# Optimization experiments

Measured on AMD Instinct MI355X. Metric: run time of the kernel, lower is better.

The kernel has to match this reference:

```python
import jax, jax.numpy as jnp
import numpy as np
from jax import lax

V, E, T, F, K = 100000, 300, 50, 100, 3
B, S = 32, 512


def setup_inputs() -> dict:
    key = jax.random.key(0)
    ks = jax.random.split(key, 10)
    inp = {
        "x": jax.random.randint(ks[0], (B, S), 0, V),
        "tags": jax.random.randint(ks[1], (B, S), 0, T),
        "emb": jax.random.normal(ks[2], (V, E), dtype=jnp.float32),
        "conv_w": jax.random.normal(ks[3], (F, E, K), dtype=jnp.float32) / np.sqrt(E * K),
        "conv_b": jnp.zeros((F,), dtype=jnp.float32),
        "fc_w": jax.random.normal(ks[4], (T, F), dtype=jnp.float32) / np.sqrt(F),
        "fc_b": jnp.zeros((T,), dtype=jnp.float32),
        "start_trans": jax.random.uniform(ks[5], (T,), dtype=jnp.float32, minval=-0.1, maxval=0.1),
        "end_trans": jax.random.uniform(ks[6], (T,), dtype=jnp.float32, minval=-0.1, maxval=0.1),
        "trans": jax.random.uniform(ks[7], (T, T), dtype=jnp.float32, minval=-0.1, maxval=0.1),
    }
    return inp


def _emissions(x, emb, conv_w, conv_b, fc_w, fc_b):
    e = emb[x]                                   # [B,S,E] embedding gather
    e = jnp.transpose(e, (0, 2, 1))              # [B,E,S]
    h = lax.conv_general_dilated(e, conv_w, (1,), [(K // 2, K // 2)])  # [B,F,S] (NCW/OIW)
    h = jax.nn.relu(h + conv_b[None, :, None])   # dropout is identity in eval
    feat = jnp.transpose(h, (0, 2, 1))           # [B,S,F]
    return (jnp.einsum("bsf,tf->bst", feat, fc_w) + fc_b).astype(jnp.float32)  # [B,S,T]


def _crf_nll(emissions, tags, start_trans, end_trans, trans):
    # numerator: score of the gold tag path (full mask)
    em_tag = jnp.take_along_axis(emissions, tags[..., None], axis=-1)[..., 0]  # [B,S]
    num = (start_trans[tags[:, 0]]
           + em_tag.sum(-1)
           + trans[tags[:, :-1], tags[:, 1:]].sum(-1)
           + end_trans[tags[:, -1]])                                           # [B]

    # denominator: forward algorithm via scan over time
    alpha0 = start_trans[None, :] + emissions[:, 0]                             # [B,T]

    def step(alpha, em_t):
        # alpha: [B,T] prev scores; em_t: [B,T] emissions at t
        new = jax.nn.logsumexp(alpha[:, :, None] + trans[None] + em_t[:, None, :], axis=1)
        return new, None

    alpha, _ = lax.scan(step, alpha0, jnp.transpose(emissions[:, 1:], (1, 0, 2)))
    log_z = jax.nn.logsumexp(alpha + end_trans[None, :], axis=-1)               # [B]
    return -(num - log_z).sum()  # torchcrf default reduction='sum'; model returns -llh


def reference(x, tags, emb, conv_w, conv_b, fc_w, fc_b, start_trans, end_trans, trans):
    emissions = _emissions(x, emb, conv_w, conv_b, fc_w, fc_b)
    return _crf_nll(emissions, tags, start_trans, end_trans, trans)
```

## Files before the change

### kernel.cpp

```cpp
#include <hip/hip_runtime.h>
#include <hip/hip_bf16.h>
#include <math.h>

#define BB 32
#define SS 512
#define EE 300
#define FF 100
#define TT 50
#define CH 16
#define NC 32

typedef __attribute__((ext_vector_type(8))) short v8s;
typedef __attribute__((ext_vector_type(4))) float v4f;
#define MFMA16 __builtin_amdgcn_mfma_f32_16x16x32_bf16

#define AP 328
#define BKC 160
#define A2P 136
#define MP 72

__device__ inline unsigned short f2bf(float v) {
    unsigned u = __float_as_uint(v);
    unsigned r = u + 0x7fff + ((u >> 16) & 1);
    return (unsigned short)(r >> 16);
}
__device__ inline float bf2f(short s) {
    return __uint_as_float(((unsigned)(unsigned short)s) << 16);
}
__device__ inline v8s ldsld8(const short* p) {
    return *(const v8s*)__builtin_assume_aligned(p, 16);
}
__device__ inline void g2lds16(const void* g, void* l) {
    __builtin_amdgcn_global_load_lds(
        (const __attribute__((address_space(1))) unsigned int*)g,
        (__attribute__((address_space(3))) unsigned int*)l, 16, 0, 0);
}

__global__ void prep_kernel(const float* __restrict__ tr, const float* __restrict__ cw,
                            const float* __restrict__ fcw,
                            unsigned short* __restrict__ wB2,
                            unsigned short* __restrict__ fcwT2,
                            unsigned short* __restrict__ AT,
                            unsigned short* __restrict__ Ab)
{
    const int gid = blockIdx.x * 256 + threadIdx.x;
    const int gs  = 64 * 256;
    for (int idx = gid; idx < 6 * 128 * BKC; idx += gs) {
        int c = idx / (128 * BKC); int r = idx - c * 128 * BKC;
        int f = r / BKC; int j = r - f * BKC;
        int gk = c * BKC + j; int kk = gk / 320; int e = gk - kk * 320;
        float v = (f < FF && e < EE) ? cw[f * 900 + e * 3 + kk] : 0.f;
        wB2[idx] = f2bf(v);
    }
    for (int idx = gid; idx < 64 * A2P; idx += gs) {
        int t = idx / A2P, f = idx - t * A2P;
        float v = (t < TT && f < FF) ? fcw[t * FF + f] : 0.f;
        fcwT2[idx] = f2bf(v);
    }
    for (int idx = gid; idx < 64 * 64; idx += gs) {
        int r = idx >> 6, c2 = idx & 63;
        AT[idx] = (r < TT && c2 < TT) ? f2bf(__expf(tr[c2 * TT + r])) : 0;
        Ab[idx] = (r < TT && c2 < TT) ? f2bf(__expf(tr[r * TT + c2])) : 0;
    }
}

__global__ __launch_bounds__(256, 2) void emis_kernel(
    const int* __restrict__ x, const float* __restrict__ emb,
    const unsigned short* __restrict__ wB2, const float* __restrict__ cb,
    const unsigned short* __restrict__ fcwT2, const float* __restrict__ fcb,
    const int* __restrict__ tags,
    float* __restrict__ expem, float* __restrict__ rmv, float* __restrict__ emtag)
{
    __shared__ __align__(16) short ldsA[34 * AP];
    __shared__ __align__(16) short ldsB[128 * BKC];

    const int b   = blockIdx.y;
    const int s0  = blockIdx.x * 32;
    const int tid = threadIdx.x;
    const int wv  = tid >> 6;
    const int lane = tid & 63;
    const int col = lane & 15;
    const int q   = lane >> 4;

    for (int g = tid; g < 34 * 75; g += 256) {
        int r = g / 75, eg = g - r * 75; int e0 = eg * 4;
        int gsq = s0 - 1 + r;
        short4 o;
        if (gsq >= 0 && gsq < SS) {
            int xr = x[b * SS + gsq];
            const float4 v = *(const float4*)(emb + (size_t)xr * EE + e0);
            o = make_short4((short)f2bf(v.x), (short)f2bf(v.y),
                            (short)f2bf(v.z), (short)f2bf(v.w));
        } else o = make_short4(0, 0, 0, 0);
        *(short4*)&ldsA[r * AP + e0] = o;
    }
    if (tid < 34 * 5) {
        int r = tid / 5, c0 = 300 + (tid % 5) * 4;
        *(short4*)&ldsA[r * AP + c0] = make_short4(0, 0, 0, 0);
    }

    v4f acc[2][2];
#pragma unroll
    for (int a = 0; a < 2; ++a)
#pragma unroll
        for (int f = 0; f < 2; ++f) acc[a][f] = (v4f){0.f, 0.f, 0.f, 0.f};

    const int ftA = wv * 2, ftB = wv * 2 + 1;
    for (int ch = 0; ch < 6; ++ch) {
        const char* gsrc = (const char*)(wB2 + (size_t)ch * 128 * BKC);
#pragma unroll
        for (int it = 0; it < 10; ++it) {
            int seg = it * 4 + wv;
            g2lds16(gsrc + seg * 1024 + lane * 16, (char*)ldsB + seg * 1024);
        }
        __syncthreads();
#pragma unroll
        for (int sl = 0; sl < 5; ++sl) {
            int gk = ch * BKC + sl * 32;
            int kk = gk / 320;
            int e0 = gk - kk * 320;
            v8s a0 = ldsld8(&ldsA[(col + kk) * AP + e0 + q * 8]);
            v8s a1 = ldsld8(&ldsA[(16 + col + kk) * AP + e0 + q * 8]);
            v8s b0 = ldsld8(&ldsB[(ftA * 16 + col) * BKC + sl * 32 + q * 8]);
            v8s b1 = ldsld8(&ldsB[(ftB * 16 + col) * BKC + sl * 32 + q * 8]);
            acc[0][0] = MFMA16(a0, b0, acc[0][0], 0, 0, 0);
            acc[0][1] = MFMA16(a0, b1, acc[0][1], 0, 0, 0);
            acc[1][0] = MFMA16(a1, b0, acc[1][0], 0, 0, 0);
            acc[1][1] = MFMA16(a1, b1, acc[1][1], 0, 0, 0);
        }
        __syncthreads();
    }

    short* A2 = ldsB;
    short* B2 = ldsB + 32 * A2P;
#pragma unroll
    for (int st = 0; st < 2; ++st)
#pragma unroll
        for (int fi = 0; fi < 2; ++fi) {
            int f = (wv * 2 + fi) * 16 + col;
            float bias = (f < FF) ? cb[f] : 0.f;
#pragma unroll
            for (int rg = 0; rg < 4; ++rg) {
                int s = st * 16 + q * 4 + rg;
                float v = (f < FF) ? fmaxf(acc[st][fi][rg] + bias, 0.f) : 0.f;
                A2[s * A2P + f] = (short)f2bf(v);
            }
        }
#pragma unroll
    for (int it = 0; it < 5; ++it) {
        int seg = it * 4 + wv;
        if (seg < 17) g2lds16((const char*)fcwT2 + seg * 1024 + lane * 16,
                              (char*)B2 + seg * 1024);
    }
    __syncthreads();

    if (wv < 2) {
        v4f a2[4];
#pragma unroll
        for (int nt = 0; nt < 4; ++nt) a2[nt] = (v4f){0.f, 0.f, 0.f, 0.f};
#pragma unroll
        for (int ks = 0; ks < 4; ++ks) {
            v8s af = ldsld8(&A2[(wv * 16 + col) * A2P + ks * 32 + q * 8]);
#pragma unroll
            for (int nt = 0; nt < 4; ++nt) {
                v8s bt = ldsld8(&B2[(nt * 16 + col) * A2P + ks * 32 + q * 8]);
                a2[nt] = MFMA16(af, bt, a2[nt], 0, 0, 0);
            }
        }
        float fb0 = fcb[col], fb1 = fcb[16 + col], fb2 = fcb[32 + col];
        float fb3 = (col < 2) ? fcb[48 + col] : 0.f;
#pragma unroll
        for (int rg = 0; rg < 4; ++rg) {
            int s = s0 + wv * 16 + q * 4 + rg;
            float e0v = a2[0][rg] + fb0;
            float e1v = a2[1][rg] + fb1;
            float e2v = a2[2][rg] + fb2;
            float e3v = (col < 2) ? a2[3][rg] + fb3 : -1e30f;
            float m = fmaxf(fmaxf(e0v, e1v), fmaxf(e2v, e3v));
#pragma unroll
            for (int off = 1; off < 16; off <<= 1) m = fmaxf(m, __shfl_xor(m, off));
            int gidx = b * SS + s;
            if (col == 0) rmv[gidx] = m;
            int tg = tags[gidx];
            float* orow = expem + (size_t)gidx * TT;
            orow[col]      = __expf(e0v - m);
            orow[16 + col] = __expf(e1v - m);
            orow[32 + col] = __expf(e2v - m);
            if (col < 2) orow[48 + col] = __expf(e3v - m);
            if (tg == col)            emtag[gidx] = e0v;
            else if (tg == 16 + col)  emtag[gidx] = e1v;
            else if (tg == 32 + col)  emtag[gidx] = e2v;
            else if (col < 2 && tg == 48 + col) emtag[gidx] = e3v;
        }
    }
}

__global__ __launch_bounds__(64) void chunk_kernel(
    const float* __restrict__ expem, const unsigned short* __restrict__ AT,
    const unsigned short* __restrict__ Ab,
    unsigned short* __restrict__ R, float* __restrict__ lsR)
{
    __shared__ __align__(16) short L[2][64 * MP];
    __shared__ __align__(16) float emL[CH][64];
    const int c = blockIdx.x, b = blockIdx.y;
    const int lane = threadIdx.x;
    const int col = lane & 15, q = lane >> 4;
    const int t0 = c * CH + 1;
    const int nf = (c == NC - 1) ? (SS - 1 - (NC - 1) * CH) : CH;

    for (int idx = lane; idx < CH * 64; idx += 64) {
        int k = idx >> 6, m = idx & 63;
        float v = 0.f;
        if (m < TT && k < nf) v = expem[((size_t)(b * SS + t0 + k)) * TT + m];
        emL[k][m] = v;
    }

    v8s af[4][2];
#pragma unroll
    for (int jt = 0; jt < 4; ++jt)
#pragma unroll
        for (int kc = 0; kc < 2; ++kc)
            af[jt][kc] = *(const v8s*)(AT + (jt * 16 + col) * 64 + kc * 32 + q * 8);
    __syncthreads();

    {
        const v8s* arow = (const v8s*)(Ab + lane * 64);
#pragma unroll
        for (int g = 0; g < 8; ++g) {
            v8s a = arow[g];
            v8s o;
#pragma unroll
            for (int e = 0; e < 8; ++e)
                o[e] = (short)f2bf(bf2f(a[e]) * emL[0][g * 8 + e]);
            *(v8s*)&L[0][lane * MP + g * 8] = o;
        }
    }

    int cur = 0;
    for (int k = 1; k < nf; ++k) {
        __syncthreads();
        v8s bf[4][2];
#pragma unroll
        for (int nt = 0; nt < 4; ++nt)
#pragma unroll
            for (int kc = 0; kc < 2; ++kc)
                bf[nt][kc] = ldsld8(&L[cur][(nt * 16 + col) * MP + kc * 32 + q * 8]);
        v4f acc[4][4];
#pragma unroll
        for (int jt = 0; jt < 4; ++jt)
#pragma unroll
            for (int nt = 0; nt < 4; ++nt) {
                acc[jt][nt] = (v4f){0.f, 0.f, 0.f, 0.f};
                acc[jt][nt] = MFMA16(af[jt][0], bf[nt][0], acc[jt][nt], 0, 0, 0);
                acc[jt][nt] = MFMA16(af[jt][1], bf[nt][1], acc[jt][nt], 0, 0, 0);
            }
        if (k < nf - 1) {
#pragma unroll
            for (int jt = 0; jt < 4; ++jt) {
                const float4 em4 = *(const float4*)&emL[k][jt * 16 + q * 4];
#pragma unroll
                for (int nt = 0; nt < 4; ++nt) {
                    short4 o;
                    o.x = (short)f2bf(acc[jt][nt][0] * em4.x);
                    o.y = (short)f2bf(acc[jt][nt][1] * em4.y);
                    o.z = (short)f2bf(acc[jt][nt][2] * em4.z);
                    o.w = (short)f2bf(acc[jt][nt][3] * em4.w);
                    *(short4*)&L[cur ^ 1][(nt * 16 + col) * MP + jt * 16 + q * 4] = o;
                }
            }
            cur ^= 1;
        } else {
            float vals[4][4][4];
            float mx = 0.f;
#pragma unroll
            for (int jt = 0; jt < 4; ++jt) {
                const float4 em4 = *(const float4*)&emL[k][jt * 16 + q * 4];
#pragma unroll
                for (int nt = 0; nt < 4; ++nt) {
                    vals[jt][nt][0] = acc[jt][nt][0] * em4.x;
                    vals[jt][nt][1] = acc[jt][nt][1] * em4.y;
                    vals[jt][nt][2] = acc[jt][nt][2] * em4.z;
                    vals[jt][nt][3] = acc[jt][nt][3] * em4.w;
#pragma unroll
                    for (int r = 0; r < 4; ++r) mx = fmaxf(mx, vals[jt][nt][r]);
                }
            }
#pragma unroll
            for (int off = 1; off < 64; off <<= 1) mx = fmaxf(mx, __shfl_xor(mx, off));
            mx = fmaxf(mx, 1e-37f);
            float inv = 1.f / mx;
            unsigned short* Rc = R + ((size_t)(b * NC + c) << 12);
#pragma unroll
            for (int jt = 0; jt < 4; ++jt)
#pragma unroll
                for (int nt = 0; nt < 4; ++nt)
#pragma unroll
                    for (int r = 0; r < 4; ++r)
                        Rc[(jt * 16 + q * 4 + r) * 64 + nt * 16 + col] =
                            f2bf(vals[jt][nt][r] * inv);
            if (lane == 0) lsR[b * NC + c] = __logf(mx);
        }
    }
}

__global__ __launch_bounds__(64) void chain_kernel(
    const float* __restrict__ expem, const unsigned short* __restrict__ R,
    const float* __restrict__ lsR, const float* __restrict__ start,
    const float* __restrict__ endt, float* __restrict__ lzpart)
{
    __shared__ __align__(16) float pvec[64];
    const int b = blockIdx.x, i = threadIdx.x;

    pvec[i] = (i < TT) ? __expf(start[i]) * expem[((size_t)(b * SS)) * TT + i] : 0.f;

    const unsigned short* Rb = R + ((size_t)(b * NC) << 12);
    v8s rowb[8];
#pragma unroll
    for (int g = 0; g < 8; ++g) rowb[g] = *(const v8s*)(Rb + i * 64 + g * 8);
    float logacc = 0.f;
    __syncthreads();

    for (int c = 0; c < NC; ++c) {
        float rw[64];
#pragma unroll
        for (int g = 0; g < 8; ++g)
#pragma unroll
            for (int e = 0; e < 8; ++e) rw[g * 8 + e] = bf2f(rowb[g][e]);
        if (c + 1 < NC) {
            const unsigned short* Rn = Rb + ((size_t)(c + 1) << 12);
#pragma unroll
            for (int g = 0; g < 8; ++g) rowb[g] = *(const v8s*)(Rn + i * 64 + g * 8);
        }
        float acc = 0.f;
        const float4* pv = (const float4*)pvec;
#pragma unroll
        for (int g = 0; g < 16; ++g) {
            float4 p4 = pv[g];
            acc = fmaf(rw[g * 4 + 0], p4.x, acc);
            acc = fmaf(rw[g * 4 + 1], p4.y, acc);
            acc = fmaf(rw[g * 4 + 2], p4.z, acc);
            acc = fmaf(rw[g * 4 + 3], p4.w, acc);
        }
        float mx = acc;
#pragma unroll
        for (int off = 1; off < 64; off <<= 1) mx = fmaxf(mx, __shfl_xor(mx, off));
        mx = fmaxf(mx, 1e-37f);
        logacc += __logf(mx) + lsR[b * NC + c];
        __syncthreads();
        pvec[i] = acc * (1.f / mx);
        __syncthreads();
    }

    float sv = (i < TT) ? pvec[i] * __expf(endt[i]) : 0.f;
#pragma unroll
    for (int off = 1; off < 64; off <<= 1) sv += __shfl_xor(sv, off);
    if (i == 0) lzpart[b] = logacc + __logf(sv);
}

__global__ __launch_bounds__(256) void final_kernel(
    const float* __restrict__ emtag, const float* __restrict__ rmv,
    const int* __restrict__ tags, const float* __restrict__ tr,
    const float* __restrict__ start, const float* __restrict__ endt,
    const float* __restrict__ lzpart, float* __restrict__ out)
{
    __shared__ float redN[256], redR[256], nllsh[BB];
    const int tid = threadIdx.x;
    const int b   = tid >> 3;
    const int sl  = tid & 7;
    const int base = b * SS + sl * 64;

    float accN = 0.f, accR = 0.f;
    for (int k = 0; k < 64; ++k) {
        int s = sl * 64 + k;
        accN += emtag[base + k];
        accR += rmv[base + k];
        int tg = tags[base + k];
        if (s < SS - 1) accN += tr[tg * TT + tags[base + k + 1]];
    }
    redN[tid] = accN; redR[tid] = accR;
    __syncthreads();

    if (sl == 0) {
        float tn = 0.f, trm = 0.f;
#pragma unroll
        for (int k = 0; k < 8; ++k) { tn += redN[b * 8 + k]; trm += redR[b * 8 + k]; }
        float num = tn + start[tags[b * SS]] + endt[tags[b * SS + SS - 1]];
        float lz  = trm + lzpart[b];
        nllsh[b] = lz - num;
    }
    __syncthreads();
    if (tid < 64) {
        float v = (tid < BB) ? nllsh[tid] : 0.f;
#pragma unroll
        for (int off = 1; off < 64; off <<= 1) v += __shfl_xor(v, off);
        if (tid == 0) out[0] = v;
    }
}

extern "C" void kernel_launch(void* const* d_in, const int* in_sizes, int n_in,
                              void* d_out, int out_size, void* d_ws, size_t ws_size,
                              hipStream_t stream)
{
    const int*   x    = (const int*)d_in[0];
    const int*   tags = (const int*)d_in[1];
    const float* emb  = (const float*)d_in[2];
    const float* cw   = (const float*)d_in[3];
    const float* cb   = (const float*)d_in[4];
    const float* fcw  = (const float*)d_in[5];
    const float* fcb  = (const float*)d_in[6];
    const float* st   = (const float*)d_in[7];
    const float* en   = (const float*)d_in[8];
    const float* tr   = (const float*)d_in[9];

    unsigned short* wB2   = (unsigned short*)d_ws;
    unsigned short* fcwT2 = wB2 + 6 * 128 * BKC;
    unsigned short* ATm   = fcwT2 + 64 * A2P;
    unsigned short* Abm   = ATm + 4096;
    unsigned short* Rm    = Abm + 4096;
    float* fbase  = (float*)(Rm + (size_t)BB * NC * 4096);
    float* expem  = fbase;
    float* rmv    = expem + (size_t)BB * SS * TT;
    float* emtag  = rmv + BB * SS;
    float* lsR    = emtag + BB * SS;
    float* lzpart = lsR + BB * NC;

    prep_kernel<<<dim3(64), 256, 0, stream>>>(tr, cw, fcw, wB2, fcwT2, ATm, Abm);
    emis_kernel<<<dim3(16, BB), 256, 0, stream>>>(x, emb, wB2, cb, fcwT2, fcb,
                                                  tags, expem, rmv, emtag);
    chunk_kernel<<<dim3(NC, BB), 64, 0, stream>>>(expem, ATm, Abm, Rm, lsR);
    chain_kernel<<<dim3(BB), 64, 0, stream>>>(expem, Rm, lsR, st, en, lzpart);
    final_kernel<<<dim3(1), 256, 0, stream>>>(emtag, rmv, tags, tr, st, en,
                                              lzpart, (float*)d_out);
}
```

Measured before the change: 256.5 us.

## Double-buffer conv weights in MFMA layout and fuse numerator into chain kernel

```diff
diff --git a/kernel.cpp b/kernel.cpp
--- a/kernel.cpp
+++ b/kernel.cpp
@@ -15,8 +15,10 @@
 #define MFMA16 __builtin_amdgcn_mfma_f32_16x16x32_bf16
 
 #define AP 328
-#define BKC 160
-#define A2P 136
+#define NCH 10
+#define CKS 3
+#define CHB (128 * 96)
+#define A2P 152
 #define MP 72
 
 __device__ inline unsigned short f2bf(float v) {
@@ -45,15 +47,22 @@
 {
     const int gid = blockIdx.x * 256 + threadIdx.x;
     const int gs  = 64 * 256;
-    for (int idx = gid; idx < 6 * 128 * BKC; idx += gs) {
-        int c = idx / (128 * BKC); int r = idx - c * 128 * BKC;
-        int f = r / BKC; int j = r - f * BKC;
-        int gk = c * BKC + j; int kk = gk / 320; int e = gk - kk * 320;
-        float v = (f < FF && e < EE) ? cw[f * 900 + e * 3 + kk] : 0.f;
+    for (int idx = gid; idx < NCH * CKS * 8 * 512; idx += gs) {
+        int e = idx & 7, p = (idx >> 3) & 63, blk = idx >> 9;
+        int ch = blk / 24, rem = blk - ch * 24;
+        int sl = rem >> 3, ft = rem & 7;
+        int col = p >> 2, q = p & 3;
+        int n  = ft * 16 + col;
+        int gk = ch * 96 + sl * 32 + q * 8 + e;
+        int kk = gk / 320, ee = gk - kk * 320;
+        float v = (n < FF && ee < EE) ? cw[n * 900 + ee * 3 + kk] : 0.f;
         wB2[idx] = f2bf(v);
     }
-    for (int idx = gid; idx < 64 * A2P; idx += gs) {
-        int t = idx / A2P, f = idx - t * A2P;
+    for (int idx = gid; idx < 16 * 512; idx += gs) {
+        int e = idx & 7, p = (idx >> 3) & 63, blk = idx >> 9;
+        int ks = blk >> 2, nt = blk & 3;
+        int col = p >> 2, q = p & 3;
+        int t = nt * 16 + col, f = ks * 32 + q * 8 + e;
         float v = (t < TT && f < FF) ? fcw[t * FF + f] : 0.f;
         fcwT2[idx] = f2bf(v);
     }
@@ -72,15 +81,23 @@
     float* __restrict__ expem, float* __restrict__ rmv, float* __restrict__ emtag)
 {
     __shared__ __align__(16) short ldsA[34 * AP];
-    __shared__ __align__(16) short ldsB[128 * BKC];
-
-    const int b   = blockIdx.y;
-    const int s0  = blockIdx.x * 32;
-    const int tid = threadIdx.x;
-    const int wv  = tid >> 6;
+    __shared__ __align__(16) short ldsB[2][CHB];
+
+    const int b    = blockIdx.y;
+    const int s0   = blockIdx.x * 32;
+    const int tid  = threadIdx.x;
+    const int wv   = tid >> 6;
     const int lane = tid & 63;
-    const int col = lane & 15;
-    const int q   = lane >> 4;
+    const int col  = lane & 15;
+    const int q    = lane >> 4;
+    const int bofs = ((col << 2) | q) << 3;
+
+#pragma unroll
+    for (int it = 0; it < 6; ++it) {
+        int seg = it * 4 + wv;
+        g2lds16((const char*)wB2 + seg * 1024 + lane * 16,
+                (char*)ldsB[0] + seg * 1024);
+    }
 
     for (int g = tid; g < 34 * 75; g += 256) {
         int r = g / 75, eg = g - r * 75; int e0 = eg * 4;
@@ -98,6 +115,7 @@
         int r = tid / 5, c0 = 300 + (tid % 5) * 4;
         *(short4*)&ldsA[r * AP + c0] = make_short4(0, 0, 0, 0);
     }
+    __syncthreads();
 
     v4f acc[2][2];
 #pragma unroll
@@ -106,23 +124,26 @@
         for (int f = 0; f < 2; ++f) acc[a][f] = (v4f){0.f, 0.f, 0.f, 0.f};
 
     const int ftA = wv * 2, ftB = wv * 2 + 1;
-    for (int ch = 0; ch < 6; ++ch) {
-        const char* gsrc = (const char*)(wB2 + (size_t)ch * 128 * BKC);
-#pragma unroll
-        for (int it = 0; it < 10; ++it) {
-            int seg = it * 4 + wv;
-            g2lds16(gsrc + seg * 1024 + lane * 16, (char*)ldsB + seg * 1024);
-        }
-        __syncthreads();
-#pragma unroll
-        for (int sl = 0; sl < 5; ++sl) {
-            int gk = ch * BKC + sl * 32;
-            int kk = gk / 320;
+    for (int ch = 0; ch < NCH; ++ch) {
+        if (ch < NCH - 1) {
+            const char* g = (const char*)(wB2 + (size_t)(ch + 1) * CHB);
+            char* l = (char*)ldsB[(ch + 1) & 1];
+#pragma unroll
+            for (int it = 0; it < 6; ++it) {
+                int seg = it * 4 + wv;
+                g2lds16(g + seg * 1024 + lane * 16, l + seg * 1024);
+            }
+        }
+        const short* Bc = ldsB[ch & 1];
+#pragma unroll
+        for (int sl = 0; sl < CKS; ++sl) {
+            int gk = ch * 96 + sl * 32;
+            int kk = (gk >= 640) ? 2 : (gk >= 320 ? 1 : 0);
             int e0 = gk - kk * 320;
             v8s a0 = ldsld8(&ldsA[(col + kk) * AP + e0 + q * 8]);
             v8s a1 = ldsld8(&ldsA[(16 + col + kk) * AP + e0 + q * 8]);
-            v8s b0 = ldsld8(&ldsB[(ftA * 16 + col) * BKC + sl * 32 + q * 8]);
-            v8s b1 = ldsld8(&ldsB[(ftB * 16 + col) * BKC + sl * 32 + q * 8]);
+            v8s b0 = ldsld8(&Bc[((sl * 8 + ftA) << 9) + bofs]);
+            v8s b1 = ldsld8(&Bc[((sl * 8 + ftB) << 9) + bofs]);
             acc[0][0] = MFMA16(a0, b0, acc[0][0], 0, 0, 0);
             acc[0][1] = MFMA16(a0, b1, acc[0][1], 0, 0, 0);
             acc[1][0] = MFMA16(a1, b0, acc[1][0], 0, 0, 0);
@@ -131,8 +152,14 @@
         __syncthreads();
     }
 
-    short* A2 = ldsB;
-    short* B2 = ldsB + 32 * A2P;
+    short* A2 = ldsB[0];
+    short* B2 = ldsB[1];
+#pragma unroll
+    for (int it = 0; it < 4; ++it) {
+        int seg = it * 4 + wv;
+        g2lds16((const char*)fcwT2 + seg * 1024 + lane * 16,
+                (char*)B2 + seg * 1024);
+    }
 #pragma unroll
     for (int st = 0; st < 2; ++st)
 #pragma unroll
@@ -146,12 +173,6 @@
                 A2[s * A2P + f] = (short)f2bf(v);
             }
         }
-#pragma unroll
-    for (int it = 0; it < 5; ++it) {
-        int seg = it * 4 + wv;
-        if (seg < 17) g2lds16((const char*)fcwT2 + seg * 1024 + lane * 16,
-                              (char*)B2 + seg * 1024);
-    }
     __syncthreads();
 
     if (wv < 2) {
@@ -163,7 +184,7 @@
             v8s af = ldsld8(&A2[(wv * 16 + col) * A2P + ks * 32 + q * 8]);
 #pragma unroll
             for (int nt = 0; nt < 4; ++nt) {
-                v8s bt = ldsld8(&B2[(nt * 16 + col) * A2P + ks * 32 + q * 8]);
+                v8s bt = ldsld8(&B2[((ks * 4 + nt) << 9) + bofs]);
                 a2[nt] = MFMA16(af, bt, a2[nt], 0, 0, 0);
             }
         }
@@ -303,98 +324,97 @@
     }
 }
 
-__global__ __launch_bounds__(64) void chain_kernel(
+__global__ __launch_bounds__(256) void chain_kernel(
     const float* __restrict__ expem, const unsigned short* __restrict__ R,
     const float* __restrict__ lsR, const float* __restrict__ start,
-    const float* __restrict__ endt, float* __restrict__ lzpart)
-{
-    __shared__ __align__(16) float pvec[64];
-    const int b = blockIdx.x, i = threadIdx.x;
-
-    pvec[i] = (i < TT) ? __expf(start[i]) * expem[((size_t)(b * SS)) * TT + i] : 0.f;
-
-    const unsigned short* Rb = R + ((size_t)(b * NC) << 12);
-    v8s rowb[8];
-#pragma unroll
-    for (int g = 0; g < 8; ++g) rowb[g] = *(const v8s*)(Rb + i * 64 + g * 8);
-    float logacc = 0.f;
-    __syncthreads();
-
-    for (int c = 0; c < NC; ++c) {
-        float rw[64];
-#pragma unroll
-        for (int g = 0; g < 8; ++g)
-#pragma unroll
-            for (int e = 0; e < 8; ++e) rw[g * 8 + e] = bf2f(rowb[g][e]);
-        if (c + 1 < NC) {
-            const unsigned short* Rn = Rb + ((size_t)(c + 1) << 12);
-#pragma unroll
-            for (int g = 0; g < 8; ++g) rowb[g] = *(const v8s*)(Rn + i * 64 + g * 8);
-        }
-        float acc = 0.f;
-        const float4* pv = (const float4*)pvec;
-#pragma unroll
-        for (int g = 0; g < 16; ++g) {
-            float4 p4 = pv[g];
-            acc = fmaf(rw[g * 4 + 0], p4.x, acc);
-            acc = fmaf(rw[g * 4 + 1], p4.y, acc);
-            acc = fmaf(rw[g * 4 + 2], p4.z, acc);
-            acc = fmaf(rw[g * 4 + 3], p4.w, acc);
-        }
-        float mx = acc;
-#pragma unroll
-        for (int off = 1; off < 64; off <<= 1) mx = fmaxf(mx, __shfl_xor(mx, off));
-        mx = fmaxf(mx, 1e-37f);
-        logacc += __logf(mx) + lsR[b * NC + c];
-        __syncthreads();
-        pvec[i] = acc * (1.f / mx);
-        __syncthreads();
-    }
-
-    float sv = (i < TT) ? pvec[i] * __expf(endt[i]) : 0.f;
-#pragma unroll
-    for (int off = 1; off < 64; off <<= 1) sv += __shfl_xor(sv, off);
-    if (i == 0) lzpart[b] = logacc + __logf(sv);
-}
-
-__global__ __launch_bounds__(256) void final_kernel(
+    const float* __restrict__ endt,
     const float* __restrict__ emtag, const float* __restrict__ rmv,
     const int* __restrict__ tags, const float* __restrict__ tr,
-    const float* __restrict__ start, const float* __restrict__ endt,
-    const float* __restrict__ lzpart, float* __restrict__ out)
-{
-    __shared__ float redN[256], redR[256], nllsh[BB];
-    const int tid = threadIdx.x;
-    const int b   = tid >> 3;
-    const int sl  = tid & 7;
-    const int base = b * SS + sl * 64;
-
-    float accN = 0.f, accR = 0.f;
-    for (int k = 0; k < 64; ++k) {
-        int s = sl * 64 + k;
-        accN += emtag[base + k];
-        accR += rmv[base + k];
-        int tg = tags[base + k];
-        if (s < SS - 1) accN += tr[tg * TT + tags[base + k + 1]];
-    }
-    redN[tid] = accN; redR[tid] = accR;
+    float* __restrict__ nllpart)
+{
+    __shared__ __align__(16) float pvec[64];
+    __shared__ float red[8];
+    __shared__ float lzsh;
+    const int b = blockIdx.x, tid = threadIdx.x;
+    const int wv = tid >> 6, i = tid & 63;
+
+    if (wv == 0) {
+        pvec[i] = (i < TT) ? __expf(start[i]) * expem[((size_t)(b * SS)) * TT + i] : 0.f;
+        const unsigned short* Rb = R + ((size_t)(b * NC) << 12);
+        v8s rb[3][8];
+#pragma unroll
+        for (int pc = 0; pc < 3; ++pc)
+#pragma unroll
+            for (int g = 0; g < 8; ++g)
+                rb[pc][g] = *(const v8s*)(Rb + ((size_t)pc << 12) + i * 64 + g * 8);
+        float logacc = 0.f;
+#pragma unroll
+        for (int c = 0; c < NC; ++c) {
+            const int slot = c % 3;
+            float acc = 0.f;
+            const float4* pv = (const float4*)pvec;
+#pragma unroll
+            for (int g = 0; g < 8; ++g) {
+                v8s v = rb[slot][g];
+                float4 pA = pv[g * 2], pB = pv[g * 2 + 1];
+                acc = fmaf(bf2f(v[0]), pA.x, acc);
+                acc = fmaf(bf2f(v[1]), pA.y, acc);
+                acc = fmaf(bf2f(v[2]), pA.z, acc);
+                acc = fmaf(bf2f(v[3]), pA.w, acc);
+                acc = fmaf(bf2f(v[4]), pB.x, acc);
+                acc = fmaf(bf2f(v[5]), pB.y, acc);
+                acc = fmaf(bf2f(v[6]), pB.z, acc);
+                acc = fmaf(bf2f(v[7]), pB.w, acc);
+            }
+            if (c + 3 < NC) {
+                const unsigned short* Rn = Rb + ((size_t)(c + 3) << 12);
+#pragma unroll
+                for (int g = 0; g < 8; ++g)
+                    rb[slot][g] = *(const v8s*)(Rn + i * 64 + g * 8);
+            }
+            float mx = acc;
+#pragma unroll
+            for (int off = 1; off < 64; off <<= 1) mx = fmaxf(mx, __shfl_xor(mx, off));
+            mx = fmaxf(mx, 1e-37f);
+            logacc += __logf(mx) + lsR[b * NC + c];
+            pvec[i] = acc * (1.f / mx);
+        }
+        float sv = (i < TT) ? pvec[i] * __expf(endt[i]) : 0.f;
+#pragma unroll
+        for (int off = 1; off < 64; off <<= 1) sv += __shfl_xor(sv, off);
+        if (i == 0) lzsh = logacc + __logf(sv);
+    } else {
+        float accN = 0.f, accR = 0.f;
+        for (int s = tid - 64; s < SS; s += 192) {
+            int gi = b * SS + s;
+            accN += emtag[gi];
+            accR += rmv[gi];
+            int tg = tags[gi];
+            if (s < SS - 1) accN += tr[tg * TT + tags[gi + 1]];
+        }
+#pragma unroll
+        for (int off = 1; off < 64; off <<= 1) {
+            accN += __shfl_xor(accN, off);
+            accR += __shfl_xor(accR, off);
+        }
+        if (i == 0) { red[wv] = accN; red[4 + wv] = accR; }
+    }
     __syncthreads();
-
-    if (sl == 0) {
-        float tn = 0.f, trm = 0.f;
-#pragma unroll
-        for (int k = 0; k < 8; ++k) { tn += redN[b * 8 + k]; trm += redR[b * 8 + k]; }
+    if (tid == 0) {
+        float tn  = red[1] + red[2] + red[3];
+        float trm = red[5] + red[6] + red[7];
         float num = tn + start[tags[b * SS]] + endt[tags[b * SS + SS - 1]];
-        float lz  = trm + lzpart[b];
-        nllsh[b] = lz - num;
-    }
-    __syncthreads();
-    if (tid < 64) {
-        float v = (tid < BB) ? nllsh[tid] : 0.f;
-#pragma unroll
-        for (int off = 1; off < 64; off <<= 1) v += __shfl_xor(v, off);
-        if (tid == 0) out[0] = v;
-    }
+        nllpart[b] = trm + lzsh - num;
+    }
+}
+
+__global__ void final_kernel(const float* __restrict__ nllpart, float* __restrict__ out)
+{
+    int tid = threadIdx.x;
+    float v = (tid < BB) ? nllpart[tid] : 0.f;
+#pragma unroll
+    for (int off = 1; off < 64; off <<= 1) v += __shfl_xor(v, off);
+    if (tid == 0) out[0] = v;
 }
 
 extern "C" void kernel_launch(void* const* d_in, const int* in_sizes, int n_in,
@@ -413,22 +433,22 @@
     const float* tr   = (const float*)d_in[9];
 
     unsigned short* wB2   = (unsigned short*)d_ws;
-    unsigned short* fcwT2 = wB2 + 6 * 128 * BKC;
-    unsigned short* ATm   = fcwT2 + 64 * A2P;
+    unsigned short* fcwT2 = wB2 + NCH * CKS * 8 * 512;
+    unsigned short* ATm   = fcwT2 + 16 * 512;
     unsigned short* Abm   = ATm + 4096;
     unsigned short* Rm    = Abm + 4096;
-    float* fbase  = (float*)(Rm + (size_t)BB * NC * 4096);
-    float* expem  = fbase;
-    float* rmv    = expem + (size_t)BB * SS * TT;
-    float* emtag  = rmv + BB * SS;
-    float* lsR    = emtag + BB * SS;
-    float* lzpart = lsR + BB * NC;
+    float* fbase   = (float*)(Rm + (size_t)BB * NC * 4096);
+    float* expem   = fbase;
+    float* rmv     = expem + (size_t)BB * SS * TT;
+    float* emtag   = rmv + BB * SS;
+    float* lsR     = emtag + BB * SS;
+    float* nllpart = lsR + BB * NC;
 
     prep_kernel<<<dim3(64), 256, 0, stream>>>(tr, cw, fcw, wB2, fcwT2, ATm, Abm);
     emis_kernel<<<dim3(16, BB), 256, 0, stream>>>(x, emb, wB2, cb, fcwT2, fcb,
                                                   tags, expem, rmv, emtag);
     chunk_kernel<<<dim3(NC, BB), 64, 0, stream>>>(expem, ATm, Abm, Rm, lsR);
-    chain_kernel<<<dim3(BB), 64, 0, stream>>>(expem, Rm, lsR, st, en, lzpart);
-    final_kernel<<<dim3(1), 256, 0, stream>>>(emtag, rmv, tags, tr, st, en,
-                                              lzpart, (float*)d_out);
-}
+    chain_kernel<<<dim3(BB), 256, 0, stream>>>(expem, Rm, lsR, st, en,
+                                               emtag, rmv, tags, tr, nllpart);
+    final_kernel<<<dim3(1), 64, 0, stream>>>(nllpart, (float*)d_out);
+}
```

After: 249.8 us. -2.6%, faster.
